# Kernel optimization log

Hardware: AMD Instinct MI355X
Metric: run time of the kernel (lower is better)

The kernel has to match this reference:

```python
import jax, jax.numpy as jnp
import numpy as np


def setup_inputs() -> dict:
    key = jax.random.key(0)
    kx, kw = jax.random.split(key)
    x = jax.random.normal(kx, (32, 256, 56, 56), dtype=jnp.float32)
    weight = jax.random.uniform(kw, (256, 256, 3, 3), dtype=jnp.float32) * 0.001
    return {"x": x, "weight": weight}


def reference(x, weight):
    # --- binarize activations with straight-through estimator ---
    # forward value = sign(x); gradient flows through clamp(x, -1, 1)
    clipped_x = jnp.clip(x, -1.0, 1.0)
    bx = jax.lax.stop_gradient(jnp.sign(x) - clipped_x) + clipped_x

    # --- binarize weights (per-output-channel mean-centered, scaled sign) ---
    w = weight
    # subtract per-output-channel mean over (in_c, kh, kw)
    bw = w - jnp.mean(w.reshape(w.shape[0], -1), axis=-1)[:, None, None, None]
    # per-output-channel scaling factor = mean |bw| (detached)
    scale = jnp.mean(jnp.abs(bw), axis=(1, 2, 3), keepdims=True)
    scale = jax.lax.stop_gradient(scale)
    clipped_w = jnp.clip(bw, -1.0, 1.0)
    binary_w = jax.lax.stop_gradient(scale * jnp.sign(bw) - clipped_w) + clipped_w

    # --- conv2d, NCHW / OIHW, stride 1, padding 1 ---
    y = jax.lax.conv_general_dilated(
        bx, binary_w,
        window_strides=(1, 1),
        padding=((1, 1), (1, 1)),
        dimension_numbers=("NCHW", "OIHW", "NCHW"),
    )
    return y
```

## Files before the change

kernel.cpp:

```cpp
#include <hip/hip_runtime.h>
#include <cstdint>
#include <cstddef>

#define N_ 32
#define C_ 256
#define H_ 56
#define W_ 56

typedef int v4i __attribute__((ext_vector_type(4)));

static constexpr size_t SX_BYTES = (size_t)N_ * 58 * 68 * 256;
static constexpr size_t WB_OFF   = SX_BYTES;
static constexpr size_t WB_BYTES = 36ull * 16 * 64 * 16;
static constexpr size_t SC_OFF   = WB_OFF + WB_BYTES;

__global__ __launch_bounds__(256) void zero_halo(char* __restrict__ sx) {
    int row = blockIdx.x;
    int n   = blockIdx.y;
    v4i z = {0, 0, 0, 0};
    char* base = sx + ((size_t)n * 58 + row) * (68 * 256);
    if (row == 0 || row == 57) {
        for (int i = threadIdx.x; i < 58 * 16; i += 256)
            *(v4i*)(base + (size_t)i * 16) = z;
    } else {
        int tid = threadIdx.x;
        if (tid < 32) {
            int wpos = (tid >> 4) * 57;
            int ch   = tid & 15;
            *(v4i*)(base + ((size_t)wpos * 16 + ch) * 16) = z;
        }
    }
}

__global__ __launch_bounds__(256) void pack_x(const float* __restrict__ x,
                                              char* __restrict__ sx) {
    __shared__ float tile[64 * 65];
    __shared__ char  ob[64 * 256];
    int tid = threadIdx.x;
    int hw0 = blockIdx.x * 64;
    int n   = blockIdx.y;

    int cl   = tid >> 6, hwl = tid & 63;
    int hwl2 = tid >> 2, cq  = tid & 3;

    for (int cb = 0; cb < 4; ++cb) {
        const float* xb = x + ((size_t)n * C_ + cb * 64) * 3136 + hw0;
#pragma unroll
        for (int i = 0; i < 16; ++i) {
            int cloc = i * 4 + cl;
            tile[cloc * 65 + hwl] = xb[(size_t)cloc * 3136 + hwl];
        }
        __syncthreads();
        int words[4];
#pragma unroll
        for (int g = 0; g < 4; ++g) {
            int word = 0;
#pragma unroll
            for (int b = 0; b < 4; ++b) {
                float v = tile[(cq * 16 + g * 4 + b) * 65 + hwl2];
                int s = (v > 0.0f) - (v < 0.0f);
                word |= (s & 0xff) << (8 * b);
            }
            words[g] = word;
        }
        v4i o4 = {words[0], words[1], words[2], words[3]};
        int ch   = cb * 4 + cq;
        int slot = (ch + hwl2) & 15;
        *(v4i*)(ob + hwl2 * 256 + slot * 16) = o4;
        __syncthreads();
    }

#pragma unroll
    for (int j = 0; j < 4; ++j) {
        int i = tid + j * 256;
        int hwl3 = i >> 4, ch = i & 15;
        v4i v = *(const v4i*)(ob + hwl3 * 256 + ((ch + hwl3) & 15) * 16);
        int hw = hw0 + hwl3;
        int h = hw / 56, w = hw - h * 56;
        int slot = (ch + (w + 1)) & 15;
        *(v4i*)(sx + (((size_t)n * 58 + h + 1) * 68 + (w + 1)) * 256 + slot * 16) = v;
    }
}

__global__ __launch_bounds__(256) void pack_w(const float* __restrict__ wt,
                                              char* __restrict__ wB,
                                              float* __restrict__ scaleg) {
    __shared__ double red[256];
    int o = blockIdx.x, tid = threadIdx.x;
    const float* wo = wt + (size_t)o * 2304;

    double s = 0;
    for (int j = tid; j < 2304; j += 256) s += (double)wo[j];
    red[tid] = s;
    __syncthreads();
    for (int k = 128; k > 0; k >>= 1) {
        if (tid < k) red[tid] += red[tid + k];
        __syncthreads();
    }
    double mean = red[0] / 2304.0;
    __syncthreads();

    double s2 = 0;
    for (int j = tid; j < 2304; j += 256) s2 += fabs((double)wo[j] - mean);
    red[tid] = s2;
    __syncthreads();
    for (int k = 128; k > 0; k >>= 1) {
        if (tid < k) red[tid] += red[tid + k];
        __syncthreads();
    }
    if (tid == 0) scaleg[o] = (float)(red[0] / 2304.0);

    if (tid < 144) {
        int kiter = tid >> 2, q = tid & 3;
        int tap = kiter >> 2, cb = kiter & 3;
        int kh = tap / 3, kw = tap - kh * 3;
        int words[4];
        for (int g = 0; g < 4; ++g) {
            int word = 0;
            for (int b = 0; b < 4; ++b) {
                int c = cb * 64 + q * 16 + g * 4 + b;
                double v = (double)wo[c * 9 + kh * 3 + kw];
                int sg = (v > mean) - (v < mean);
                word |= (sg & 0xff) << (8 * b);
            }
            words[g] = word;
        }
        v4i pk = {words[0], words[1], words[2], words[3]};
        *(v4i*)(wB + (((size_t)kiter * 16 + (o >> 4)) * 64 + q * 16 + (o & 15)) * 16) = pk;
    }
}

__global__ __launch_bounds__(256, 2) void conv_mfma(const char* __restrict__ sx,
                                                    const v4i* __restrict__ wB,
                                                    const float* __restrict__ scaleg,
                                                    float* __restrict__ out) {
    __shared__ char xs[4 * 58 * 256];
    int tid = threadIdx.x;
    int wave = tid >> 6, lane = tid & 63;
    int hp = blockIdx.x, n = blockIdx.y;
    int h0 = hp * 2;

    const char* src = sx + ((size_t)n * 58 + h0) * (68 * 256);
    for (int i = tid; i < 4 * 58 * 16; i += 256) {
        int pos = i >> 4;
        int row = pos / 58;
        int w   = pos - row * 58;
        v4i v = *(const v4i*)(src + ((size_t)(row * 68 + w) << 8) + ((size_t)(i & 15) << 4));
        *(v4i*)(xs + (size_t)i * 16) = v;
    }

    int lm = lane & 15, q = lane >> 4;

    int wof[7], ro[7];
#pragma unroll
    for (int mf = 0; mf < 7; ++mf) {
        int m = mf * 16 + lm;
        int r = (m >= 56) ? 1 : 0;
        ro[mf]  = r;
        wof[mf] = m - 56 * r;
    }

    v4i acc[7][4];
#pragma unroll
    for (int mf = 0; mf < 7; ++mf)
#pragma unroll
        for (int of = 0; of < 4; ++of) { v4i z = {0, 0, 0, 0}; acc[mf][of] = z; }

    const v4i* wBw = wB + (size_t)(wave * 4) * 64 + lane;

    __syncthreads();

    v4i bA[4], bB[4], aA[7], aB[7];

#pragma unroll
    for (int of = 0; of < 4; ++of) bA[of] = wBw[of * 64];
    {
        int cbq = q;
#pragma unroll
        for (int mf = 0; mf < 7; ++mf) {
            int win  = wof[mf];
            int pos  = ro[mf] * 58 + win;
            int phys = (pos << 4) | ((cbq + win) & 15);
            aA[mf] = *(const v4i*)(xs + ((size_t)phys << 4));
        }
    }

    for (int k2 = 0; k2 < 18; ++k2) {
        int k0 = 2 * k2, k1 = k0 + 1;
#pragma unroll
        for (int of = 0; of < 4; ++of) bB[of] = wBw[(size_t)k1 * 1024 + of * 64];
        {
            int tap = k1 >> 2, cb = k1 & 3;
            int dh = tap / 3, dw = tap - dh * 3;
            int cbq = cb * 4 + q;
#pragma unroll
            for (int mf = 0; mf < 7; ++mf) {
                int win  = wof[mf] + dw;
                int pos  = (dh + ro[mf]) * 58 + win;
                int phys = (pos << 4) | ((cbq + win) & 15);
                aB[mf] = *(const v4i*)(xs + ((size_t)phys << 4));
            }
        }
#pragma unroll
        for (int mf = 0; mf < 7; ++mf)
#pragma unroll
            for (int of = 0; of < 4; ++of)
                acc[mf][of] = __builtin_amdgcn_mfma_i32_16x16x64_i8(
                    aA[mf], bA[of], acc[mf][of], 0, 0, 0);
        if (k2 < 17) {
            int kn = k0 + 2;
#pragma unroll
            for (int of = 0; of < 4; ++of) bA[of] = wBw[(size_t)kn * 1024 + of * 64];
            int tap = kn >> 2, cb = kn & 3;
            int dh = tap / 3, dw = tap - dh * 3;
            int cbq = cb * 4 + q;
#pragma unroll
            for (int mf = 0; mf < 7; ++mf) {
                int win  = wof[mf] + dw;
                int pos  = (dh + ro[mf]) * 58 + win;
                int phys = (pos << 4) | ((cbq + win) & 15);
                aA[mf] = *(const v4i*)(xs + ((size_t)phys << 4));
            }
        }
#pragma unroll
        for (int mf = 0; mf < 7; ++mf)
#pragma unroll
            for (int of = 0; of < 4; ++of)
                acc[mf][of] = __builtin_amdgcn_mfma_i32_16x16x64_i8(
                    aB[mf], bB[of], acc[mf][of], 0, 0, 0);
    }

#pragma unroll
    for (int of = 0; of < 4; ++of) {
        int o = (wave * 4 + of) * 16 + lm;
        float s = scaleg[o];
#pragma unroll
        for (int mf = 0; mf < 7; ++mf) {
            int m  = mf * 16 + q * 4;
            int r  = (m >= 56) ? 1 : 0;
            int wb = m - 56 * r;
            float* ob = out + ((size_t)(n * C_ + o) * H_ + h0 + r) * W_ + wb;
            float4 v = {s * (float)acc[mf][of].x, s * (float)acc[mf][of].y,
                        s * (float)acc[mf][of].z, s * (float)acc[mf][of].w};
            *(float4*)ob = v;
        }
    }
}

extern "C" void kernel_launch(void* const* d_in, const int* in_sizes, int n_in,
                              void* d_out, int out_size, void* d_ws, size_t ws_size,
                              hipStream_t stream) {
    const float* x   = (const float*)d_in[0];
    const float* wgt = (const float*)d_in[1];
    float* out = (float*)d_out;
    char* ws = (char*)d_ws;

    char*  sx = ws;
    char*  wb = ws + WB_OFF;
    float* sg = (float*)(ws + SC_OFF);

    zero_halo<<<dim3(58, N_), dim3(256), 0, stream>>>(sx);
    pack_x<<<dim3(49, N_), dim3(256), 0, stream>>>(x, sx);
    pack_w<<<dim3(256), dim3(256), 0, stream>>>(wgt, wb, sg);
    conv_mfma<<<dim3(28, N_), dim3(256), 0, stream>>>(sx, (const v4i*)wb, sg, out);
}
```

Baseline: 248.2 us.

## Enlarge conv tile to four rows, stage via LDS DMA, fold halo zeroing

The conv kernel now processes four output rows per 512-thread block, so each staged input slab (6 rows) serves more outputs and halo re-reads drop. The LDS fill switches to global_load_lds direct transfers. Each wave starts its K loop at a staggered offset to spread LDS bank and weight-load traffic. MFMA sections are bracketed with s_setprio. Separately, halo zeroing is merged into pack_x as extra blocks, and the x loads are vectorised to float4. The larger block and register footprint may lower occupancy.

```diff
diff --git a/kernel.cpp b/kernel.cpp
--- a/kernel.cpp
+++ b/kernel.cpp
@@ -8,47 +8,56 @@
 #define W_ 56
 
 typedef int v4i __attribute__((ext_vector_type(4)));
+typedef uint32_t __attribute__((address_space(1))) glb_u32;
+typedef uint32_t __attribute__((address_space(3))) lds_u32;
 
 static constexpr size_t SX_BYTES = (size_t)N_ * 58 * 68 * 256;
 static constexpr size_t WB_OFF   = SX_BYTES;
 static constexpr size_t WB_BYTES = 36ull * 16 * 64 * 16;
 static constexpr size_t SC_OFF   = WB_OFF + WB_BYTES;
 
-__global__ __launch_bounds__(256) void zero_halo(char* __restrict__ sx) {
-    int row = blockIdx.x;
+__global__ __launch_bounds__(256) void pack_x(const float* __restrict__ x,
+                                              char* __restrict__ sx) {
+    int tid = threadIdx.x;
     int n   = blockIdx.y;
     v4i z = {0, 0, 0, 0};
-    char* base = sx + ((size_t)n * 58 + row) * (68 * 256);
-    if (row == 0 || row == 57) {
-        for (int i = threadIdx.x; i < 58 * 16; i += 256)
-            *(v4i*)(base + (size_t)i * 16) = z;
-    } else {
-        int tid = threadIdx.x;
-        if (tid < 32) {
-            int wpos = (tid >> 4) * 57;
-            int ch   = tid & 15;
-            *(v4i*)(base + ((size_t)wpos * 16 + ch) * 16) = z;
-        }
-    }
-}
-
-__global__ __launch_bounds__(256) void pack_x(const float* __restrict__ x,
-                                              char* __restrict__ sx) {
+
+    if (blockIdx.x >= 49) {
+        if (blockIdx.x == 49) {
+            for (int i = tid; i < 2 * 58 * 16; i += 256) {
+                int r   = i / (58 * 16);
+                int rem = i - r * (58 * 16);
+                char* base = sx + ((size_t)n * 58 + (size_t)r * 57) * (68 * 256);
+                *(v4i*)(base + (size_t)rem * 16) = z;
+            }
+        } else {
+            for (int i = tid; i < 56 * 32; i += 256) {
+                int r = 1 + (i >> 5);
+                int c = i & 31;
+                int wpos = (c >> 4) * 57, ch = c & 15;
+                *(v4i*)(sx + (((size_t)n * 58 + r) * 68 + wpos) * 256 + ch * 16) = z;
+            }
+        }
+        return;
+    }
+
     __shared__ float tile[64 * 65];
     __shared__ char  ob[64 * 256];
-    int tid = threadIdx.x;
     int hw0 = blockIdx.x * 64;
-    int n   = blockIdx.y;
-
-    int cl   = tid >> 6, hwl = tid & 63;
+
+    int c16 = tid >> 4, hw4 = tid & 15;
     int hwl2 = tid >> 2, cq  = tid & 3;
 
     for (int cb = 0; cb < 4; ++cb) {
         const float* xb = x + ((size_t)n * C_ + cb * 64) * 3136 + hw0;
 #pragma unroll
-        for (int i = 0; i < 16; ++i) {
-            int cloc = i * 4 + cl;
-            tile[cloc * 65 + hwl] = xb[(size_t)cloc * 3136 + hwl];
+        for (int j = 0; j < 4; ++j) {
+            int cloc = j * 16 + c16;
+            float4 v = *(const float4*)(xb + (size_t)cloc * 3136 + hw4 * 4);
+            tile[cloc * 65 + hw4 * 4 + 0] = v.x;
+            tile[cloc * 65 + hw4 * 4 + 1] = v.y;
+            tile[cloc * 65 + hw4 * 4 + 2] = v.z;
+            tile[cloc * 65 + hw4 * 4 + 3] = v.w;
         }
         __syncthreads();
         int words[4];
@@ -130,34 +139,42 @@
     }
 }
 
-__global__ __launch_bounds__(256, 2) void conv_mfma(const char* __restrict__ sx,
+__device__ __forceinline__ void stage_chunk(const char* src, char* xs, int i) {
+    int pos = i >> 4;
+    int row = (pos * 1130) >> 16;
+    int w   = pos - row * 58;
+    const char* g = src + (((size_t)(row * 68 + w)) << 8) + ((size_t)(i & 15) << 4);
+    char* l = xs + (size_t)i * 16;
+    __builtin_amdgcn_global_load_lds((const glb_u32*)g, (lds_u32*)l, 16, 0, 0);
+}
+
+__global__ __launch_bounds__(512, 2) void conv_mfma(const char* __restrict__ sx,
                                                     const v4i* __restrict__ wB,
                                                     const float* __restrict__ scaleg,
                                                     float* __restrict__ out) {
-    __shared__ char xs[4 * 58 * 256];
+    __shared__ char xs[6 * 58 * 256];
     int tid = threadIdx.x;
     int wave = tid >> 6, lane = tid & 63;
-    int hp = blockIdx.x, n = blockIdx.y;
-    int h0 = hp * 2;
+    int hq = blockIdx.x, n = blockIdx.y;
+    int h0 = hq * 4;
 
     const char* src = sx + ((size_t)n * 58 + h0) * (68 * 256);
-    for (int i = tid; i < 4 * 58 * 16; i += 256) {
-        int pos = i >> 4;
-        int row = pos / 58;
-        int w   = pos - row * 58;
-        v4i v = *(const v4i*)(src + ((size_t)(row * 68 + w) << 8) + ((size_t)(i & 15) << 4));
-        *(v4i*)(xs + (size_t)i * 16) = v;
-    }
+#pragma unroll
+    for (int it = 0; it < 10; ++it) stage_chunk(src, xs, tid + it * 512);
+    if (tid < 448) stage_chunk(src, xs, tid + 5120);
 
     int lm = lane & 15, q = lane >> 4;
-
-    int wof[7], ro[7];
+    int og = wave & 3, mg = wave >> 2;
+    int kstart = __builtin_amdgcn_readfirstlane((9 * wave) >> 1);
+
+    int posb[7], slotb[7];
 #pragma unroll
     for (int mf = 0; mf < 7; ++mf) {
-        int m = mf * 16 + lm;
-        int r = (m >= 56) ? 1 : 0;
-        ro[mf]  = r;
-        wof[mf] = m - 56 * r;
+        int m = mg * 112 + mf * 16 + lm;
+        int r = m / 56;
+        int wof = m - r * 56;
+        posb[mf]  = r * 58 + wof;
+        slotb[mf] = q + wof;
     }
 
     v4i acc[7][4];
@@ -166,79 +183,73 @@
 #pragma unroll
         for (int of = 0; of < 4; ++of) { v4i z = {0, 0, 0, 0}; acc[mf][of] = z; }
 
-    const v4i* wBw = wB + (size_t)(wave * 4) * 64 + lane;
+    const v4i* wBw = wB + (size_t)(og * 4) * 64 + lane;
 
     __syncthreads();
 
     v4i bA[4], bB[4], aA[7], aB[7];
 
-#pragma unroll
-    for (int of = 0; of < 4; ++of) bA[of] = wBw[of * 64];
-    {
-        int cbq = q;
+    auto loadB = [&](int k, v4i* b) {
+#pragma unroll
+        for (int of = 0; of < 4; ++of) b[of] = wBw[(size_t)k * 1024 + of * 64];
+    };
+    auto loadA = [&](int k, v4i* a) {
+        int tap = k >> 2, cb = k & 3;
+        int dh = (tap * 11) >> 5;
+        int dw = tap - dh * 3;
+        int pofs = dh * 58 + dw;
+        int sofs = cb * 4 + dw;
 #pragma unroll
         for (int mf = 0; mf < 7; ++mf) {
-            int win  = wof[mf];
-            int pos  = ro[mf] * 58 + win;
-            int phys = (pos << 4) | ((cbq + win) & 15);
-            aA[mf] = *(const v4i*)(xs + ((size_t)phys << 4));
-        }
-    }
-
-    for (int k2 = 0; k2 < 18; ++k2) {
-        int k0 = 2 * k2, k1 = k0 + 1;
-#pragma unroll
-        for (int of = 0; of < 4; ++of) bB[of] = wBw[(size_t)k1 * 1024 + of * 64];
+            int pos  = posb[mf] + pofs;
+            int slot = (slotb[mf] + sofs) & 15;
+            a[mf] = *(const v4i*)(xs + ((size_t)pos << 8) + ((size_t)slot << 4));
+        }
+    };
+    auto wrap = [&](int t) { int k = kstart + t; return k >= 36 ? k - 36 : k; };
+
+    loadB(kstart, bA);
+    loadA(kstart, aA);
+
+    for (int t2 = 0; t2 < 18; ++t2) {
+        int ta = 2 * t2;
         {
-            int tap = k1 >> 2, cb = k1 & 3;
-            int dh = tap / 3, dw = tap - dh * 3;
-            int cbq = cb * 4 + q;
-#pragma unroll
-            for (int mf = 0; mf < 7; ++mf) {
-                int win  = wof[mf] + dw;
-                int pos  = (dh + ro[mf]) * 58 + win;
-                int phys = (pos << 4) | ((cbq + win) & 15);
-                aB[mf] = *(const v4i*)(xs + ((size_t)phys << 4));
-            }
-        }
+            int kb = wrap(ta + 1);
+            loadB(kb, bB);
+            loadA(kb, aB);
+        }
+        __builtin_amdgcn_s_setprio(1);
 #pragma unroll
         for (int mf = 0; mf < 7; ++mf)
 #pragma unroll
             for (int of = 0; of < 4; ++of)
                 acc[mf][of] = __builtin_amdgcn_mfma_i32_16x16x64_i8(
                     aA[mf], bA[of], acc[mf][of], 0, 0, 0);
-        if (k2 < 17) {
-            int kn = k0 + 2;
-#pragma unroll
-            for (int of = 0; of < 4; ++of) bA[of] = wBw[(size_t)kn * 1024 + of * 64];
-            int tap = kn >> 2, cb = kn & 3;
-            int dh = tap / 3, dw = tap - dh * 3;
-            int cbq = cb * 4 + q;
-#pragma unroll
-            for (int mf = 0; mf < 7; ++mf) {
-                int win  = wof[mf] + dw;
-                int pos  = (dh + ro[mf]) * 58 + win;
-                int phys = (pos << 4) | ((cbq + win) & 15);
-                aA[mf] = *(const v4i*)(xs + ((size_t)phys << 4));
-            }
-        }
+        __builtin_amdgcn_s_setprio(0);
+        if (t2 < 17) {
+            int kc = wrap(ta + 2);
+            loadB(kc, bA);
+            loadA(kc, aA);
+        }
+        __builtin_amdgcn_s_setprio(1);
 #pragma unroll
         for (int mf = 0; mf < 7; ++mf)
 #pragma unroll
             for (int of = 0; of < 4; ++of)
                 acc[mf][of] = __builtin_amdgcn_mfma_i32_16x16x64_i8(
                     aB[mf], bB[of], acc[mf][of], 0, 0, 0);
+        __builtin_amdgcn_s_setprio(0);
     }
 
 #pragma unroll
     for (int of = 0; of < 4; ++of) {
-        int o = (wave * 4 + of) * 16 + lm;
+        int o = og * 64 + of * 16 + lm;
         float s = scaleg[o];
 #pragma unroll
         for (int mf = 0; mf < 7; ++mf) {
-            int m  = mf * 16 + q * 4;
-            int r  = (m >= 56) ? 1 : 0;
-            int wb = m - 56 * r;
+            int m  = mg * 112 + mf * 16 + q * 4;
+            int r  = m / 56;
+            int wb = m - r * 56;
             float* ob = out + ((size_t)(n * C_ + o) * H_ + h0 + r) * W_ + wb;
             float4 v = {s * (float)acc[mf][of].x, s * (float)acc[mf][of].y,
                         s * (float)acc[mf][of].z, s * (float)acc[mf][of].w};
@@ -259,8 +270,7 @@
     char*  wb = ws + WB_OFF;
     float* sg = (float*)(ws + SC_OFF);
 
-    zero_halo<<<dim3(58, N_), dim3(256), 0, stream>>>(sx);
-    pack_x<<<dim3(49, N_), dim3(256), 0, stream>>>(x, sx);
+    pack_x<<<dim3(51, N_), dim3(256), 0, stream>>>(x, sx);
     pack_w<<<dim3(256), dim3(256), 0, stream>>>(wgt, wb, sg);
-    conv_mfma<<<dim3(28, N_), dim3(256), 0, stream>>>(sx, (const v4i*)wb, sg, out);
-}
+    conv_mfma<<<dim3(14, N_), dim3(512), 0, stream>>>(sx, (const v4i*)wb, sg, out);
+}
```

Result: no change. 251.8 us (+1.4%).
